# Optimization experiments

Measured on AMD Instinct MI355X. Metric: run time of the kernel, lower is better.

The kernel has to match this reference:

```python
import jax, jax.numpy as jnp
import numpy as np

DIM = 384
WH, WW = 7, 7
N_HEADS = 12
HEAD_DIM = DIM // N_HEADS
SCALE = HEAD_DIM ** -0.5


def _relative_position_index(Wh, Ww):
    coords = np.stack(np.meshgrid(np.arange(Wh), np.arange(Ww), indexing='ij'))  # (2,Wh,Ww)
    cf = coords.reshape(2, -1)                       # (2, N)
    rc = cf[:, :, None] - cf[:, None, :]             # (2, N, N)
    rc = rc.transpose(1, 2, 0).copy()                # (N, N, 2)
    rc[..., 0] += Wh - 1
    rc[..., 1] += Ww - 1
    rc[..., 0] *= 2 * Ww - 1
    return jnp.asarray(rc.sum(-1))                   # (N, N) int

REL_IDX = _relative_position_index(WH, WW)


def setup_inputs() -> dict:
    key = jax.random.key(0)
    ks = jax.random.split(key, 5)
    B_, N, C = 4096, WH * WW, DIM
    nW = 64
    x = jax.random.normal(ks[0], (B_, N, C), dtype=jnp.float32)
    mask = jnp.zeros((nW, N, N), dtype=jnp.float32)  # 0/-inf additive mask; zeros = no shift
    qkv_w = jax.random.normal(ks[1], (3 * C, C), dtype=jnp.float32) * (C ** -0.5)
    qkv_b = jnp.zeros((3 * C,), dtype=jnp.float32)
    proj_w = jax.random.normal(ks[2], (C, C), dtype=jnp.float32) * (C ** -0.5)
    proj_b = jnp.zeros((C,), dtype=jnp.float32)
    rpb_table = jax.random.normal(ks[3], ((2 * WH - 1) * (2 * WW - 1), N_HEADS), dtype=jnp.float32) * 0.02
    return {"x": x, "mask": mask, "qkv_w": qkv_w, "qkv_b": qkv_b,
            "proj_w": proj_w, "proj_b": proj_b, "rpb_table": rpb_table}


def reference(x, mask, qkv_w, qkv_b, proj_w, proj_b, rpb_table):
    B_, N, C = x.shape
    H, hd = N_HEADS, HEAD_DIM
    # qkv projection -> (3, B_, H, N, hd)
    qkv = (x @ qkv_w.T + qkv_b).reshape(B_, N, 3, H, hd).transpose(2, 0, 3, 1, 4)
    q, k, v = qkv[0] * SCALE, qkv[1], qkv[2]
    attn = jnp.einsum('bhnd,bhmd->bhnm', q, k)                       # (B_, H, N, N)
    rpb = rpb_table[REL_IDX.reshape(-1)].reshape(N, N, H).transpose(2, 0, 1)  # (H, N, N)
    attn = attn + rpb[None]
    nW = mask.shape[0]
    attn = attn.reshape(B_ // nW, nW, H, N, N) + mask[None, :, None]
    attn = attn.reshape(B_, H, N, N)
    attn = jax.nn.softmax(attn, axis=-1)
    out = jnp.einsum('bhnm,bhmd->bhnd', attn, v)                     # (B_, H, N, hd)
    out = out.transpose(0, 2, 1, 3).reshape(B_, N, C)
    return out @ proj_w.T + proj_b
```

## Files before the change

### kernel.cpp

```cpp
#include <hip/hip_runtime.h>
#include <stdint.h>


typedef unsigned short u16;
typedef short short8 __attribute__((ext_vector_type(8)));
typedef float f32x4 __attribute__((ext_vector_type(4)));

static __device__ __forceinline__ u16 f2bf(float f) {
  unsigned u = __builtin_bit_cast(unsigned, f);
  return (u16)((u + 0x7fffu + ((u >> 16) & 1u)) >> 16);
}

static __device__ __forceinline__ unsigned cvt_pk_bf16(float a, float b) {
  unsigned r;
  asm("v_cvt_pk_bf16_f32 %0, %1, %2" : "=v"(r) : "v"(a), "v"(b));
  return r;
}

static __device__ __forceinline__ void async_cp16(const u16* g, u16* l) {
  __builtin_amdgcn_global_load_lds(
      (__attribute__((address_space(1))) unsigned int*)g,
      (__attribute__((address_space(3))) unsigned int*)l, 16, 0, 0);
}

__global__ __launch_bounds__(256) void prep_kernel(
    const float* __restrict__ x, const float* __restrict__ wq,
    const float* __restrict__ wp, const float* __restrict__ rpt,
    const float* __restrict__ qb,
    u16* __restrict__ xb, u16* __restrict__ wqb, u16* __restrict__ wpb,
    float* __restrict__ rpbf, float* __restrict__ bias_s)
{
  const int bid = blockIdx.x, tid = threadIdx.x;
  const float S = 0.17677669529663687f;
  if (bid < 1024) {
    const float4* x4 = (const float4*)x;
    ushort4* o4 = (ushort4*)xb;
    for (unsigned i = bid * 256u + tid; i < 19267584u; i += 262144u) {
      float4 v = x4[i];
      ushort4 o; o.x = f2bf(v.x); o.y = f2bf(v.y); o.z = f2bf(v.z); o.w = f2bf(v.w);
      o4[i] = o;
    }
  } else if (bid < 1088) {
    for (unsigned i = (bid - 1024) * 256u + tid; i < 147456u; i += 16384u) {
      if (i < 110592u) {
        float4 v = ((const float4*)wq)[i];
        const float s = (i < 36864u) ? S : 1.0f;
        ushort4 o; o.x = f2bf(v.x * s); o.y = f2bf(v.y * s);
        o.z = f2bf(v.z * s); o.w = f2bf(v.w * s);
        ((ushort4*)wqb)[i] = o;
      } else {
        unsigned k = i - 110592u;
        float4 v = ((const float4*)wp)[k];
        ushort4 o; o.x = f2bf(v.x); o.y = f2bf(v.y); o.z = f2bf(v.z); o.w = f2bf(v.w);
        ((ushort4*)wpb)[k] = o;
      }
    }
  } else {
    for (int e = (bid - 1088) * 256 + tid; e < 28812 + 1152; e += 2048) {
      if (e < 28812) {
        int h = e / 2401, r2 = e - h * 2401;
        int i = r2 / 49, j = r2 - (r2 / 49) * 49;
        int rel = (i / 7 - j / 7 + 6) * 13 + (i % 7 - j % 7 + 6);
        rpbf[e] = rpt[rel * 12 + h];
      } else {
        int c = e - 28812;
        bias_s[c] = qb[c] * ((c < 384) ? S : 1.0f);
      }
    }
  }
}

template <int MODE>
__global__ __launch_bounds__(256) void gemm_nt(
    const u16* __restrict__ A, const u16* __restrict__ Bw,
    const float* __restrict__ bias, void* __restrict__ Cp)
{
  constexpr int NTOT = (MODE == 0) ? 1152 : 384;
  constexpr int NX = NTOT / 128;
  constexpr int CPX = (NX * 1568) / 8;
  __shared__ u16 smem[16384];

  const int tid = threadIdx.x;
  const int wave = tid >> 6, lane = tid & 63;
  const int lr = lane & 15, quad = lane >> 4;

  const int lid = (blockIdx.x & 7) * CPX + (blockIdx.x >> 3);
  const int by = lid / NX;
  const int bx = lid - by * NX;
  const int m0 = by * 128, n0 = bx * 128;
  const int wm = (wave & 1) * 64, wn = (wave >> 1) * 64;

  const int r4 = tid >> 2;
  const int cs = ((tid & 3) ^ ((r4 >> 1) & 3)) * 8;
  const size_t ga0 = (size_t)(m0 + r4) * 384 + cs;
  const size_t ga1 = (size_t)(m0 + 64 + r4) * 384 + cs;
  const size_t gb0 = (size_t)(n0 + r4) * 384 + cs;
  const size_t gb1 = (size_t)(n0 + 64 + r4) * 384 + cs;

  f32x4 acc[4][4] = {};
  const int sw = (lr >> 1) & 3;

  {
    u16* As = smem; u16* Bs = smem + 4096;
    async_cp16(&A[ga0], As + wave * 512);
    async_cp16(&A[ga1], As + 2048 + wave * 512);
    async_cp16(&Bw[gb0], Bs + wave * 512);
    async_cp16(&Bw[gb1], Bs + 2048 + wave * 512);
  }
  __syncthreads();

  int buf = 0;
#pragma unroll 2
  for (int it = 0; it < 12; ++it) {
    u16* As = smem + buf * 8192;
    u16* Bs = As + 4096;
    if (it < 11) {
      u16* An = smem + (buf ^ 1) * 8192;
      u16* Bn = An + 4096;
      const int k0 = (it + 1) * 32;
      async_cp16(&A[ga0 + k0], An + wave * 512);
      async_cp16(&A[ga1 + k0], An + 2048 + wave * 512);
      async_cp16(&Bw[gb0 + k0], Bn + wave * 512);
      async_cp16(&Bw[gb1 + k0], Bn + 2048 + wave * 512);
    }
    short8 af[4], bf[4];
#pragma unroll
    for (int mi = 0; mi < 4; ++mi)
      af[mi] = *(const short8*)&As[(wm + mi * 16 + lr) * 32 + ((quad ^ sw) * 8)];
#pragma unroll
    for (int ni = 0; ni < 4; ++ni)
      bf[ni] = *(const short8*)&Bs[(wn + ni * 16 + lr) * 32 + ((quad ^ sw) * 8)];
#pragma unroll
    for (int mi = 0; mi < 4; ++mi)
#pragma unroll
      for (int ni = 0; ni < 4; ++ni)
        acc[mi][ni] = __builtin_amdgcn_mfma_f32_16x16x32_bf16(af[mi], bf[ni], acc[mi][ni], 0, 0, 0);
    __syncthreads();
    buf ^= 1;
  }

  float bv[4];
#pragma unroll
  for (int ni = 0; ni < 4; ++ni) bv[ni] = bias[n0 + wn + ni * 16 + lr];

  if (MODE == 0) {
    u16* ot = smem;
#pragma unroll
    for (int mi = 0; mi < 4; ++mi)
#pragma unroll
      for (int ni = 0; ni < 4; ++ni) {
        const int row0 = wm + mi * 16 + quad * 4;
        const int col = wn + ni * 16 + lr;
        const int slot = (col >> 3) ^ ((row0 >> 2) & 7);
        u16* dst = &ot[row0 * 128 + slot * 8 + (col & 7)];
        const unsigned p01 = cvt_pk_bf16(acc[mi][ni][0] + bv[ni], acc[mi][ni][1] + bv[ni]);
        const unsigned p23 = cvt_pk_bf16(acc[mi][ni][2] + bv[ni], acc[mi][ni][3] + bv[ni]);
        dst[0]   = (u16)p01; dst[128] = (u16)(p01 >> 16);
        dst[256] = (u16)p23; dst[384] = (u16)(p23 >> 16);
      }
    __syncthreads();
    u16* outp = (u16*)Cp;
#pragma unroll
    for (int j = 0; j < 8; ++j) {
      const int cid = j * 256 + tid;
      const int row = cid >> 4, slot = cid & 15;
      const int c8 = slot ^ ((row >> 2) & 7);
      *(short8*)&outp[(size_t)(m0 + row) * NTOT + n0 + c8 * 8] =
          *(const short8*)&ot[row * 128 + slot * 8];
    }
  } else {
    float* fl = (float*)smem;
    float* outp = (float*)Cp;
#pragma unroll
    for (int h = 0; h < 2; ++h) {
      if ((wave & 1) == h) {
#pragma unroll
        for (int mi = 0; mi < 4; ++mi)
#pragma unroll
          for (int ni = 0; ni < 4; ++ni)
#pragma unroll
            for (int r = 0; r < 4; ++r) {
              const int lrow = mi * 16 + quad * 4 + r;
              const int col = wn + ni * 16 + lr;
              const int slot = (col >> 2) ^ ((lrow >> 2) & 7);
              fl[lrow * 128 + slot * 4 + (col & 3)] = acc[mi][ni][r] + bv[ni];
            }
      }
      __syncthreads();
#pragma unroll
      for (int j = 0; j < 8; ++j) {
        const int cid = j * 256 + tid;
        const int lrow = cid >> 5, slot = cid & 31;
        const int c4 = slot ^ ((lrow >> 2) & 7);
        *(f32x4*)&outp[(size_t)(m0 + h * 64 + lrow) * NTOT + n0 + c4 * 4] =
            *(const f32x4*)&fl[lrow * 128 + slot * 4];
      }
      if (h == 0) __syncthreads();
    }
  }
}

__global__ __launch_bounds__(256) void attn_kernel(
    const u16* __restrict__ qkv, const float* __restrict__ mask,
    const float* __restrict__ rpbf, u16* __restrict__ attnout)
{
  __shared__ u16 P_lds[4][64 * 64];
  __shared__ u16 VT_lds[4][32 * 64];
  const int tid = threadIdx.x;
  const int wave = tid >> 6, lane = tid & 63;
  const int lr = lane & 15, quad = lane >> 4;
  const int bl = (blockIdx.x & 7) * 1536 + (blockIdx.x >> 3);
  const int b = bl / 3;
  const int h = (bl - b * 3) * 4 + wave;

  const size_t base = (size_t)b * (49 * 1152);
  u16* P  = P_lds[wave];
  u16* Vt = VT_lds[wave];
  const short8 z8 = {0, 0, 0, 0, 0, 0, 0, 0};

  {
    const int dh = lane & 3;
    const int tk0 = lane >> 2;
#pragma unroll
    for (int p = 0; p < 4; ++p) {
      const int tok = p * 16 + tk0;
      short8 v = z8;
      if (tok < 49)
        v = *(const short8*)&qkv[base + (size_t)tok * 1152 + 768 + h * 32 + dh * 8];
#pragma unroll
      for (int j = 0; j < 8; ++j) {
        const int d = dh * 8 + j;
        Vt[d * 64 + (((tok >> 3) ^ j) * 8) + (tok & 7)] = ((const u16*)&v)[j];
      }
    }
  }

  short8 qf[4], kf[4];
#pragma unroll
  for (int mi = 0; mi < 4; ++mi) {
    const int row = mi * 16 + lr;
    qf[mi] = (row < 49)
        ? *(const short8*)&qkv[base + (size_t)row * 1152 + h * 32 + quad * 8] : z8;
  }
#pragma unroll
  for (int ni = 0; ni < 4; ++ni) {
    const int tok = ni * 16 + lr;
    kf[ni] = (tok < 49)
        ? *(const short8*)&qkv[base + (size_t)tok * 1152 + 384 + h * 32 + quad * 8] : z8;
  }
  f32x4 s[4][4] = {};
#pragma unroll
  for (int mi = 0; mi < 4; ++mi)
#pragma unroll
    for (int ni = 0; ni < 4; ++ni)
      s[mi][ni] = __builtin_amdgcn_mfma_f32_16x16x32_bf16(qf[mi], kf[ni], s[mi][ni], 0, 0, 0);

  const float* rh = &rpbf[h * 2401];
  const float* mw = &mask[(size_t)(b & 63) * 2401];
  float linv[4][4];
#pragma unroll
  for (int mi = 0; mi < 4; ++mi) {
#pragma unroll
    for (int r = 0; r < 4; ++r) {
      const int row = mi * 16 + quad * 4 + r;
      float vals[4];
#pragma unroll
      for (int ni = 0; ni < 4; ++ni) {
        const int col = ni * 16 + lr;
        float v;
        if (row < 49 && col < 49)
          v = s[mi][ni][r] + rh[row * 49 + col] + mw[row * 49 + col];
        else
          v = -1e30f;
        vals[ni] = v;
      }
      float m = fmaxf(fmaxf(vals[0], vals[1]), fmaxf(vals[2], vals[3]));
      m = fmaxf(m, __shfl_xor(m, 1));
      m = fmaxf(m, __shfl_xor(m, 2));
      m = fmaxf(m, __shfl_xor(m, 4));
      m = fmaxf(m, __shfl_xor(m, 8));
      float l = 0.f;
#pragma unroll
      for (int ni = 0; ni < 4; ++ni) {
        const float p = __expf(vals[ni] - m);
        l += p;
        const int col = ni * 16 + lr;
        P[row * 64 + (((col >> 3) ^ (row & 7)) * 8) + (col & 7)] = f2bf(p);
      }
      l += __shfl_xor(l, 1);
      l += __shfl_xor(l, 2);
      l += __shfl_xor(l, 4);
      l += __shfl_xor(l, 8);
      linv[mi][r] = 1.0f / l;
    }
  }

  f32x4 o[4][2] = {};
#pragma unroll
  for (int kh = 0; kh < 2; ++kh) {
    const int chunk = (kh * 4 + quad) ^ (lr & 7);
    short8 vf[2];
#pragma unroll
    for (int ni = 0; ni < 2; ++ni)
      vf[ni] = *(const short8*)&Vt[(ni * 16 + lr) * 64 + chunk * 8];
#pragma unroll
    for (int mi = 0; mi < 4; ++mi) {
      short8 pf = *(const short8*)&P[(mi * 16 + lr) * 64 + chunk * 8];
#pragma unroll
      for (int ni = 0; ni < 2; ++ni)
        o[mi][ni] = __builtin_amdgcn_mfma_f32_16x16x32_bf16(pf, vf[ni], o[mi][ni], 0, 0, 0);
    }
  }

  u16* outp = attnout + (size_t)b * (49 * 384) + h * 32;
#pragma unroll
  for (int mi = 0; mi < 4; ++mi)
#pragma unroll
    for (int r = 0; r < 4; ++r) {
      const int row = mi * 16 + quad * 4 + r;
      if (row < 49) {
        const float li = linv[mi][r];
#pragma unroll
        for (int ni = 0; ni < 2; ++ni)
          outp[row * 384 + ni * 16 + lr] = f2bf(o[mi][ni][r] * li);
      }
    }
}

extern "C" void kernel_launch(void* const* d_in, const int* in_sizes, int n_in,
                              void* d_out, int out_size, void* d_ws, size_t ws_size,
                              hipStream_t stream) {
  const float* x      = (const float*)d_in[0];
  const float* mask   = (const float*)d_in[1];
  const float* qkv_w  = (const float*)d_in[2];
  const float* qkv_b  = (const float*)d_in[3];
  const float* proj_w = (const float*)d_in[4];
  const float* proj_b = (const float*)d_in[5];
  const float* rpb_t  = (const float*)d_in[6];
  float* out = (float*)d_out;

  char* ws = (char*)d_ws;
  u16* qkv    = (u16*)ws;
  u16* xb     = (u16*)(ws + 462422016u);
  u16* attnout = xb;
  u16* wqb    = (u16*)(ws + 462422016u + 154140672u);
  u16* wpb    = wqb + 442368;
  float* rpbf = (float*)((char*)wpb + 294912u);
  float* bias_s = (float*)((char*)rpbf + 115248u);

  prep_kernel<<<1096, 256, 0, stream>>>(x, qkv_w, proj_w, rpb_t, qkv_b,
                                        xb, wqb, wpb, rpbf, bias_s);
  gemm_nt<0><<<14112, 256, 0, stream>>>(xb, wqb, bias_s, (void*)qkv);
  attn_kernel<<<12288, 256, 0, stream>>>(qkv, mask, rpbf, attnout);
  gemm_nt<1><<<4704, 256, 0, stream>>>(attnout, wpb, proj_b, (void*)out);
}
```

Baseline: 1.165 ms.

## Enlarge GEMM block tile to 256x128 with 512 threads

Both GEMMs now use 512-thread blocks, each computing a 256x128 output tile with eight waves in a 4x2 arrangement, so every staged B tile is shared by twice as many rows. This halves the grid size and cuts redundant global and L2 loads of the weight tile per output element. LDS use rises to 48KB per block, and the epilogue is split into more synchronized passes, which may reduce occupancy and add barrier overhead.

```diff
diff --git a/kernel.cpp b/kernel.cpp
--- a/kernel.cpp
+++ b/kernel.cpp
@@ -71,65 +71,59 @@
 }
 
 template <int MODE>
-__global__ __launch_bounds__(256) void gemm_nt(
+__global__ __launch_bounds__(512, 4) void gemm_nt(
     const u16* __restrict__ A, const u16* __restrict__ Bw,
     const float* __restrict__ bias, void* __restrict__ Cp)
 {
   constexpr int NTOT = (MODE == 0) ? 1152 : 384;
   constexpr int NX = NTOT / 128;
-  constexpr int CPX = (NX * 1568) / 8;
-  __shared__ u16 smem[16384];
+  constexpr int CPX = (NX * 784) / 8;
+  __shared__ u16 smem[24576];
 
   const int tid = threadIdx.x;
   const int wave = tid >> 6, lane = tid & 63;
   const int lr = lane & 15, quad = lane >> 4;
+  const int wr = wave >> 1, wc = wave & 1;
 
   const int lid = (blockIdx.x & 7) * CPX + (blockIdx.x >> 3);
   const int by = lid / NX;
   const int bx = lid - by * NX;
-  const int m0 = by * 128, n0 = bx * 128;
-  const int wm = (wave & 1) * 64, wn = (wave >> 1) * 64;
-
-  const int r4 = tid >> 2;
-  const int cs = ((tid & 3) ^ ((r4 >> 1) & 3)) * 8;
-  const size_t ga0 = (size_t)(m0 + r4) * 384 + cs;
-  const size_t ga1 = (size_t)(m0 + 64 + r4) * 384 + cs;
-  const size_t gb0 = (size_t)(n0 + r4) * 384 + cs;
-  const size_t gb1 = (size_t)(n0 + 64 + r4) * 384 + cs;
+  const int m0 = by * 256, n0 = bx * 128;
+
+  const int r = tid >> 2;
+  const int cs = ((tid & 3) ^ ((r >> 1) & 3)) * 8;
+  const size_t ga0 = (size_t)(m0 + r) * 384 + cs;
+  const size_t ga1 = (size_t)(m0 + 128 + r) * 384 + cs;
+  const size_t gb0 = (size_t)(n0 + r) * 384 + cs;
+
+#define STAGE(BUF, K0)                                                  \
+  {                                                                     \
+    u16* As_ = smem + (BUF) * 12288;                                    \
+    u16* Bs_ = As_ + 8192;                                              \
+    async_cp16(&A[ga0 + (K0)], As_ + wave * 512);                       \
+    async_cp16(&A[ga1 + (K0)], As_ + 4096 + wave * 512);                \
+    async_cp16(&Bw[gb0 + (K0)], Bs_ + wave * 512);                      \
+  }
 
   f32x4 acc[4][4] = {};
   const int sw = (lr >> 1) & 3;
 
-  {
-    u16* As = smem; u16* Bs = smem + 4096;
-    async_cp16(&A[ga0], As + wave * 512);
-    async_cp16(&A[ga1], As + 2048 + wave * 512);
-    async_cp16(&Bw[gb0], Bs + wave * 512);
-    async_cp16(&Bw[gb1], Bs + 2048 + wave * 512);
-  }
+  STAGE(0, 0)
   __syncthreads();
 
   int buf = 0;
 #pragma unroll 2
   for (int it = 0; it < 12; ++it) {
-    u16* As = smem + buf * 8192;
-    u16* Bs = As + 4096;
-    if (it < 11) {
-      u16* An = smem + (buf ^ 1) * 8192;
-      u16* Bn = An + 4096;
-      const int k0 = (it + 1) * 32;
-      async_cp16(&A[ga0 + k0], An + wave * 512);
-      async_cp16(&A[ga1 + k0], An + 2048 + wave * 512);
-      async_cp16(&Bw[gb0 + k0], Bn + wave * 512);
-      async_cp16(&Bw[gb1 + k0], Bn + 2048 + wave * 512);
-    }
+    u16* As = smem + buf * 12288;
+    u16* Bs = As + 8192;
+    if (it < 11) STAGE(buf ^ 1, (it + 1) * 32)
     short8 af[4], bf[4];
 #pragma unroll
     for (int mi = 0; mi < 4; ++mi)
-      af[mi] = *(const short8*)&As[(wm + mi * 16 + lr) * 32 + ((quad ^ sw) * 8)];
+      af[mi] = *(const short8*)&As[(wr * 64 + mi * 16 + lr) * 32 + ((quad ^ sw) * 8)];
 #pragma unroll
     for (int ni = 0; ni < 4; ++ni)
-      bf[ni] = *(const short8*)&Bs[(wn + ni * 16 + lr) * 32 + ((quad ^ sw) * 8)];
+      bf[ni] = *(const short8*)&Bs[(wc * 64 + ni * 16 + lr) * 32 + ((quad ^ sw) * 8)];
 #pragma unroll
     for (int mi = 0; mi < 4; ++mi)
 #pragma unroll
@@ -141,63 +135,70 @@
 
   float bv[4];
 #pragma unroll
-  for (int ni = 0; ni < 4; ++ni) bv[ni] = bias[n0 + wn + ni * 16 + lr];
+  for (int ni = 0; ni < 4; ++ni) bv[ni] = bias[n0 + wc * 64 + ni * 16 + lr];
 
   if (MODE == 0) {
     u16* ot = smem;
-#pragma unroll
-    for (int mi = 0; mi < 4; ++mi)
-#pragma unroll
-      for (int ni = 0; ni < 4; ++ni) {
-        const int row0 = wm + mi * 16 + quad * 4;
-        const int col = wn + ni * 16 + lr;
-        const int slot = (col >> 3) ^ ((row0 >> 2) & 7);
-        u16* dst = &ot[row0 * 128 + slot * 8 + (col & 7)];
-        const unsigned p01 = cvt_pk_bf16(acc[mi][ni][0] + bv[ni], acc[mi][ni][1] + bv[ni]);
-        const unsigned p23 = cvt_pk_bf16(acc[mi][ni][2] + bv[ni], acc[mi][ni][3] + bv[ni]);
-        dst[0]   = (u16)p01; dst[128] = (u16)(p01 >> 16);
-        dst[256] = (u16)p23; dst[384] = (u16)(p23 >> 16);
-      }
-    __syncthreads();
     u16* outp = (u16*)Cp;
 #pragma unroll
-    for (int j = 0; j < 8; ++j) {
-      const int cid = j * 256 + tid;
-      const int row = cid >> 4, slot = cid & 15;
-      const int c8 = slot ^ ((row >> 2) & 7);
-      *(short8*)&outp[(size_t)(m0 + row) * NTOT + n0 + c8 * 8] =
-          *(const short8*)&ot[row * 128 + slot * 8];
+    for (int p = 0; p < 2; ++p) {
+      if ((wr >> 1) == p) {
+#pragma unroll
+        for (int mi = 0; mi < 4; ++mi)
+#pragma unroll
+          for (int ni = 0; ni < 4; ++ni) {
+            const int row_l = (wr & 1) * 64 + mi * 16 + quad * 4;
+            const int col = wc * 64 + ni * 16 + lr;
+            const int slot = (col >> 3) ^ ((row_l >> 2) & 7);
+            u16* dst = &ot[row_l * 128 + slot * 8 + (col & 7)];
+            const unsigned p01 = cvt_pk_bf16(acc[mi][ni][0] + bv[ni], acc[mi][ni][1] + bv[ni]);
+            const unsigned p23 = cvt_pk_bf16(acc[mi][ni][2] + bv[ni], acc[mi][ni][3] + bv[ni]);
+            dst[0]   = (u16)p01; dst[128] = (u16)(p01 >> 16);
+            dst[256] = (u16)p23; dst[384] = (u16)(p23 >> 16);
+          }
+      }
+      __syncthreads();
+#pragma unroll
+      for (int j = 0; j < 4; ++j) {
+        const int cid = j * 512 + tid;
+        const int row_l = cid >> 4, slot = cid & 15;
+        const int c8 = slot ^ ((row_l >> 2) & 7);
+        *(short8*)&outp[(size_t)(m0 + p * 128 + row_l) * NTOT + n0 + c8 * 8] =
+            *(const short8*)&ot[row_l * 128 + slot * 8];
+      }
+      if (p == 0) __syncthreads();
     }
   } else {
     float* fl = (float*)smem;
     float* outp = (float*)Cp;
 #pragma unroll
-    for (int h = 0; h < 2; ++h) {
-      if ((wave & 1) == h) {
+    for (int p = 0; p < 4; ++p) {
+      if (wr == p) {
 #pragma unroll
         for (int mi = 0; mi < 4; ++mi)
 #pragma unroll
           for (int ni = 0; ni < 4; ++ni)
 #pragma unroll
-            for (int r = 0; r < 4; ++r) {
-              const int lrow = mi * 16 + quad * 4 + r;
-              const int col = wn + ni * 16 + lr;
+            for (int rr = 0; rr < 4; ++rr) {
+              const int lrow = mi * 16 + quad * 4 + rr;
+              const int col = wc * 64 + ni * 16 + lr;
               const int slot = (col >> 2) ^ ((lrow >> 2) & 7);
-              fl[lrow * 128 + slot * 4 + (col & 3)] = acc[mi][ni][r] + bv[ni];
+              fl[lrow * 128 + slot * 4 + (col & 3)] = acc[mi][ni][rr] + bv[ni];
             }
       }
       __syncthreads();
 #pragma unroll
-      for (int j = 0; j < 8; ++j) {
-        const int cid = j * 256 + tid;
+      for (int j = 0; j < 4; ++j) {
+        const int cid = j * 512 + tid;
         const int lrow = cid >> 5, slot = cid & 31;
         const int c4 = slot ^ ((lrow >> 2) & 7);
-        *(f32x4*)&outp[(size_t)(m0 + h * 64 + lrow) * NTOT + n0 + c4 * 4] =
+        *(f32x4*)&outp[(size_t)(m0 + p * 64 + lrow) * NTOT + n0 + c4 * 4] =
             *(const f32x4*)&fl[lrow * 128 + slot * 4];
       }
-      if (h == 0) __syncthreads();
-    }
-  }
+      if (p < 3) __syncthreads();
+    }
+  }
+#undef STAGE
 }
 
 __global__ __launch_bounds__(256) void attn_kernel(
@@ -350,7 +351,7 @@
 
   prep_kernel<<<1096, 256, 0, stream>>>(x, qkv_w, proj_w, rpb_t, qkv_b,
                                         xb, wqb, wpb, rpbf, bias_s);
-  gemm_nt<0><<<14112, 256, 0, stream>>>(xb, wqb, bias_s, (void*)qkv);
+  gemm_nt<0><<<7056, 512, 0, stream>>>(xb, wqb, bias_s, (void*)qkv);
   attn_kernel<<<12288, 256, 0, stream>>>(qkv, mask, rpbf, attnout);
-  gemm_nt<1><<<4704, 256, 0, stream>>>(attnout, wpb, proj_b, (void*)out);
-}
+  gemm_nt<1><<<2352, 512, 0, stream>>>(attnout, wpb, proj_b, (void*)out);
+}
```

New measurement: 1.135 ms. 1.03x faster.
